# Optimization experiments

Hardware: AMD Instinct MI355X
Metric: run time of the kernel (lower is better)

The kernel has to match this reference:

```python
import jax, jax.numpy as jnp
import numpy as np

GROUP_SIZE = 128  # cfg.group_size

def dequantize_int4(weight_q, scale, zero_point, group_size):
    # weight_q: (out, in) int values in [0,15]; scale/zero_point: (out, n_groups)
    out_f, in_f = weight_q.shape
    n_groups = in_f // group_size
    w = weight_q.astype(jnp.float32).reshape(out_f, n_groups, group_size)
    w = (w - zero_point[:, :, None]) * scale[:, :, None]
    return w.reshape(out_f, in_f)

def setup_inputs() -> dict:
    key = jax.random.key(0)
    k1, k2, k3, k4, k5 = jax.random.split(key, 5)
    B, S, D_IN, D_OUT = 2, 2048, 4096, 4096
    n_groups = D_IN // GROUP_SIZE
    x = jax.random.normal(k1, (B, S, D_IN), dtype=jnp.float32)
    weight_q = jax.random.randint(k2, (D_OUT, D_IN), 0, 16, dtype=jnp.int32)
    scale = jax.random.uniform(k3, (D_OUT, n_groups), dtype=jnp.float32, minval=0.001, maxval=0.02)
    zero_point = jax.random.uniform(k4, (D_OUT, n_groups), dtype=jnp.float32, minval=0.0, maxval=15.0)
    bias = jax.random.normal(k5, (D_OUT,), dtype=jnp.float32)
    return {"x": x, "weight_q": weight_q, "scale": scale, "zero_point": zero_point, "bias": bias}

def reference(x, weight_q, scale, zero_point, bias):
    # Faithful to QuantizedLinear.forward with bits=4: dequantize then F.linear
    w = dequantize_int4(weight_q, scale, zero_point, GROUP_SIZE).astype(x.dtype)  # (out, in)
    return jnp.einsum('bsi,oi->bso', x, w) + bias
```

## Files before the change

### kernel.cpp

```cpp
#include <hip/hip_runtime.h>

typedef __bf16 bf16x8 __attribute__((ext_vector_type(8)));
typedef float f32x4 __attribute__((ext_vector_type(4)));

__device__ __forceinline__ void gload16(const void* g, void* l) {
    __builtin_amdgcn_global_load_lds(
        (const __attribute__((address_space(1))) unsigned int*)g,
        (__attribute__((address_space(3))) unsigned int*)l, 16, 0, 0);
}

__global__ void k_convert_x(const float* __restrict__ x, __bf16* __restrict__ xb, size_t n) {
    size_t i = ((size_t)blockIdx.x * blockDim.x + threadIdx.x) * 8;
    if (i >= n) return;
    const float4 a = *(const float4*)(x + i);
    const float4 b = *(const float4*)(x + i + 4);
    bf16x8 v;
    v[0] = (__bf16)a.x; v[1] = (__bf16)a.y; v[2] = (__bf16)a.z; v[3] = (__bf16)a.w;
    v[4] = (__bf16)b.x; v[5] = (__bf16)b.y; v[6] = (__bf16)b.z; v[7] = (__bf16)b.w;
    *(bf16x8*)(xb + i) = v;
}

__global__ void k_dequant_w(const int* __restrict__ wq, const float* __restrict__ scale,
                            const float* __restrict__ zp, __bf16* __restrict__ wb,
                            int K, int GS, int NG) {
    size_t i = ((size_t)blockIdx.x * blockDim.x + threadIdx.x) * 8;
    int o = (int)(i / K);
    int k = (int)(i % K);
    int g = k / GS;
    float s = scale[(size_t)o * NG + g];
    float z = zp[(size_t)o * NG + g];
    const int4 q0 = *(const int4*)(wq + i);
    const int4 q1 = *(const int4*)(wq + i + 4);
    bf16x8 v;
    v[0] = (__bf16)(((float)q0.x - z) * s); v[1] = (__bf16)(((float)q0.y - z) * s);
    v[2] = (__bf16)(((float)q0.z - z) * s); v[3] = (__bf16)(((float)q0.w - z) * s);
    v[4] = (__bf16)(((float)q1.x - z) * s); v[5] = (__bf16)(((float)q1.y - z) * s);
    v[6] = (__bf16)(((float)q1.z - z) * s); v[7] = (__bf16)(((float)q1.w - z) * s);
    *(bf16x8*)(wb + i) = v;
}

#define BKg 32
#define TILEB 32768
#define ATILEB 16384

__global__ __launch_bounds__(512, 2) void k_gemm256(
    const __bf16* __restrict__ A, const __bf16* __restrict__ B,
    const float* __restrict__ bias, float* __restrict__ C,
    int M, int N, int K)
{
    __shared__ __align__(16) char lds[4 * TILEB];
    const int tid = threadIdx.x;
    const int w = tid >> 6, lane = tid & 63;
    const int wm = w >> 2, wn = w & 3;
    const int lr = lane & 15, hi = lane >> 4;
    const int NT = K / BKg;

    const int nbx = N / 256;
    const int nwg = nbx * (M / 256);
    const int bid = (int)blockIdx.x;
    const int q = nwg >> 3, r = nwg & 7;
    const int xcd = bid & 7, loc = bid >> 3;
    const int swz = (xcd < r ? xcd * (q + 1) : r * (q + 1) + (xcd - r) * q) + loc;
    const int m0 = (swz / nbx) * 256;
    const int n0 = (swz % nbx) * 256;

    size_t aOff[2], bOff[2];
#pragma unroll
    for (int L = 0; L < 2; ++L) {
        int c = L * 512 + tid;
        int row = c >> 2, ch = (c & 3) ^ ((c >> 3) & 3);
        aOff[L] = (size_t)(m0 + row) * K + ch * 8;
        bOff[L] = (size_t)(n0 + row) * K + ch * 8;
    }
    int dstOff[2];
#pragma unroll
    for (int L = 0; L < 2; ++L) dstOff[L] = (L * 512 + w * 64) * 16;

    const int chR = (hi ^ ((lr >> 1) & 3)) * 16;
    const int aRd = (wm * 128 + lr) * 64 + chR;
    const int bRd = ATILEB + (wn * 64 + lr) * 64 + chR;

#define STAGE_A(tt, buf) do {                                              \
    const int kk_ = (tt) * BKg;                                            \
    gload16(A + aOff[0] + kk_, lds + (buf) * TILEB + dstOff[0]);           \
    gload16(A + aOff[1] + kk_, lds + (buf) * TILEB + dstOff[1]);           \
} while (0)
#define STAGE_B(tt, buf) do {                                              \
    const int kk_ = (tt) * BKg;                                            \
    gload16(B + bOff[0] + kk_, lds + (buf) * TILEB + ATILEB + dstOff[0]);  \
    gload16(B + bOff[1] + kk_, lds + (buf) * TILEB + ATILEB + dstOff[1]);  \
} while (0)
#define RD_A(dst, buf, m) dst = *(const bf16x8*)(lds + (buf) * TILEB + aRd + (m) * 1024)
#define RD_B(dst, buf, n) dst = *(const bf16x8*)(lds + (buf) * TILEB + bRd + (n) * 1024)

    f32x4 acc[8][4] = {};
    bf16x8 aF0[8], bF0[4], aF1[8], bF1[4];

    STAGE_A(0, 0); STAGE_B(0, 0);
    STAGE_A(1, 1); STAGE_B(1, 1);
    STAGE_A(2, 2); STAGE_B(2, 2);
    asm volatile("s_waitcnt vmcnt(8)" ::: "memory");
    __builtin_amdgcn_s_barrier();
    RD_A(aF0[0], 0, 0); RD_A(aF0[1], 0, 1); RD_A(aF0[2], 0, 2);
    RD_A(aF0[3], 0, 3); RD_A(aF0[4], 0, 4); RD_A(aF0[5], 0, 5);

#define ITER(t, AC, BC, AN) do {                                            \
    const int bt = (t) & 3, bt1 = ((t) + 1) & 3, bt3 = ((t) + 3) & 3;       \
    int t3 = (t) + 3; if (t3 >= NT) t3 -= NT;                               \
    RD_A(AC[6], bt, 6); RD_A(AC[7], bt, 7);                                 \
    RD_B(BC[0], bt, 0); RD_B(BC[1], bt, 1);                                 \
    RD_B(BC[2], bt, 2); RD_B(BC[3], bt, 3);                                 \
    STAGE_A(t3, bt3);                                                       \
    asm volatile("s_waitcnt vmcnt(6)" ::: "memory");                        \
    __builtin_amdgcn_s_barrier();                                           \
    asm volatile("s_waitcnt lgkmcnt(0)" ::: "memory");                      \
    __builtin_amdgcn_sched_barrier(0);                                      \
    __builtin_amdgcn_s_setprio(1);                                          \
    _Pragma("unroll")                                                       \
    for (int m_ = 0; m_ < 4; ++m_)                                          \
        _Pragma("unroll")                                                   \
        for (int n_ = 0; n_ < 4; ++n_)                                      \
            acc[m_][n_] = __builtin_amdgcn_mfma_f32_16x16x32_bf16(          \
                AC[m_], BC[n_], acc[m_][n_], 0, 0, 0);                      \
    __builtin_amdgcn_s_setprio(0);                                          \
    __builtin_amdgcn_s_barrier();                                           \
    if ((t) + 1 < NT) {                                                     \
        RD_A(AN[0], bt1, 0); RD_A(AN[1], bt1, 1); RD_A(AN[2], bt1, 2);      \
        RD_A(AN[3], bt1, 3); RD_A(AN[4], bt1, 4); RD_A(AN[5], bt1, 5);      \
    }                                                                       \
    STAGE_B(t3, bt3);                                                       \
    __builtin_amdgcn_s_barrier();                                           \
    asm volatile("s_waitcnt lgkmcnt(0)" ::: "memory");                      \
    __builtin_amdgcn_sched_barrier(0);                                      \
    __builtin_amdgcn_s_setprio(1);                                          \
    _Pragma("unroll")                                                       \
    for (int m_ = 4; m_ < 8; ++m_)                                          \
        _Pragma("unroll")                                                   \
        for (int n_ = 0; n_ < 4; ++n_)                                      \
            acc[m_][n_] = __builtin_amdgcn_mfma_f32_16x16x32_bf16(          \
                AC[m_], BC[n_], acc[m_][n_], 0, 0, 0);                      \
    __builtin_amdgcn_s_setprio(0);                                          \
    __builtin_amdgcn_s_barrier();                                           \
} while (0)

    for (int t = 0; t < NT; t += 2) {
        ITER(t,     aF0, bF0, aF1);
        ITER(t + 1, aF1, bF1, aF0);
    }

#pragma unroll
    for (int n_ = 0; n_ < 4; ++n_) {
        const int col = n0 + wn * 64 + n_ * 16 + lr;
        const float bv = bias[col];
#pragma unroll
        for (int m_ = 0; m_ < 8; ++m_) {
            const size_t rbase = (size_t)(m0 + wm * 128 + m_ * 16 + hi * 4) * N + col;
            C[rbase]               = acc[m_][n_][0] + bv;
            C[rbase + N]           = acc[m_][n_][1] + bv;
            C[rbase + 2 * (size_t)N] = acc[m_][n_][2] + bv;
            C[rbase + 3 * (size_t)N] = acc[m_][n_][3] + bv;
        }
    }
#undef ITER
#undef STAGE_A
#undef STAGE_B
#undef RD_A
#undef RD_B
}

template <int MODE>
__global__ __launch_bounds__(256, 2) void k_gemm(
    const __bf16* __restrict__ Ab, const float* __restrict__ Af,
    const __bf16* __restrict__ Bb, const int* __restrict__ Bq,
    const float* __restrict__ scale, const float* __restrict__ zp,
    const float* __restrict__ bias, float* __restrict__ C,
    int M, int N, int K, int NG, int GS)
{
    __shared__ __align__(16) __bf16 As[128 * 32];
    __shared__ __align__(16) __bf16 Bs[128 * 32];

    const int tid  = threadIdx.x;
    const int w    = tid >> 6;
    const int lane = tid & 63;
    const int wm   = w >> 1, wn = w & 1;
    const int m0   = blockIdx.y * 128, n0 = blockIdx.x * 128;
    const int lr   = lane & 15;
    const int lc   = lane >> 4;

    f32x4 acc[4][4] = {};

    for (int kk = 0; kk < K; kk += 32) {
        if constexpr (MODE == 0) {
#pragma unroll
            for (int i = 0; i < 2; i++) {
                int c = i * 256 + tid;
                const __bf16* g = Ab + (size_t)(m0 + (c >> 2)) * K + kk + (c & 3) * 8;
                gload16(g, (char*)As + (i * 256 + w * 64) * 16);
            }
        } else {
            int row = tid >> 1, half = tid & 1;
            const float* g = Af + (size_t)(m0 + row) * K + kk + half * 16;
            float4 f0 = *(const float4*)g;
            float4 f1 = *(const float4*)(g + 4);
            float4 f2 = *(const float4*)(g + 8);
            float4 f3 = *(const float4*)(g + 12);
            bf16x8 v0, v1;
            v0[0] = (__bf16)f0.x; v0[1] = (__bf16)f0.y; v0[2] = (__bf16)f0.z; v0[3] = (__bf16)f0.w;
            v0[4] = (__bf16)f1.x; v0[5] = (__bf16)f1.y; v0[6] = (__bf16)f1.z; v0[7] = (__bf16)f1.w;
            v1[0] = (__bf16)f2.x; v1[1] = (__bf16)f2.y; v1[2] = (__bf16)f2.z; v1[3] = (__bf16)f2.w;
            v1[4] = (__bf16)f3.x; v1[5] = (__bf16)f3.y; v1[6] = (__bf16)f3.z; v1[7] = (__bf16)f3.w;
            *(bf16x8*)(As + row * 32 + half * 16)     = v0;
            *(bf16x8*)(As + row * 32 + half * 16 + 8) = v1;
        }
        if constexpr (MODE <= 1) {
#pragma unroll
            for (int i = 0; i < 2; i++) {
                int c = i * 256 + tid;
                const __bf16* g = Bb + (size_t)(n0 + (c >> 2)) * K + kk + (c & 3) * 8;
                gload16(g, (char*)Bs + (i * 256 + w * 64) * 16);
            }
        } else {
            int row = tid >> 1, half = tid & 1;
            int o = n0 + row;
            int kbase = kk + half * 16;
            int g = kbase / GS;
            float s = scale[(size_t)o * NG + g];
            float z = zp[(size_t)o * NG + g];
            const int* qp = Bq + (size_t)o * K + kbase;
            int4 q0 = *(const int4*)qp;
            int4 q1 = *(const int4*)(qp + 4);
            int4 q2 = *(const int4*)(qp + 8);
            int4 q3 = *(const int4*)(qp + 12);
            bf16x8 v0, v1;
            v0[0] = (__bf16)(((float)q0.x - z) * s); v0[1] = (__bf16)(((float)q0.y - z) * s);
            v0[2] = (__bf16)(((float)q0.z - z) * s); v0[3] = (__bf16)(((float)q0.w - z) * s);
            v0[4] = (__bf16)(((float)q1.x - z) * s); v0[5] = (__bf16)(((float)q1.y - z) * s);
            v0[6] = (__bf16)(((float)q1.z - z) * s); v0[7] = (__bf16)(((float)q1.w - z) * s);
            v1[0] = (__bf16)(((float)q2.x - z) * s); v1[1] = (__bf16)(((float)q2.y - z) * s);
            v1[2] = (__bf16)(((float)q2.z - z) * s); v1[3] = (__bf16)(((float)q2.w - z) * s);
            v1[4] = (__bf16)(((float)q3.x - z) * s); v1[5] = (__bf16)(((float)q3.y - z) * s);
            v1[6] = (__bf16)(((float)q3.z - z) * s); v1[7] = (__bf16)(((float)q3.w - z) * s);
            *(bf16x8*)(Bs + row * 32 + half * 16)     = v0;
            *(bf16x8*)(Bs + row * 32 + half * 16 + 8) = v1;
        }

        __syncthreads();

        bf16x8 af[4], bfm[4];
#pragma unroll
        for (int a = 0; a < 4; a++)
            af[a] = *(const bf16x8*)(As + (wm * 64 + a * 16 + lr) * 32 + lc * 8);
#pragma unroll
        for (int b = 0; b < 4; b++)
            bfm[b] = *(const bf16x8*)(Bs + (wn * 64 + b * 16 + lr) * 32 + lc * 8);
#pragma unroll
        for (int a = 0; a < 4; a++)
#pragma unroll
            for (int b = 0; b < 4; b++)
                acc[a][b] = __builtin_amdgcn_mfma_f32_16x16x32_bf16(af[a], bfm[b], acc[a][b], 0, 0, 0);

        __syncthreads();
    }

#pragma unroll
    for (int b = 0; b < 4; b++) {
        int col = n0 + wn * 64 + b * 16 + lr;
        float bv = bias[col];
#pragma unroll
        for (int a = 0; a < 4; a++) {
            int rbase = m0 + wm * 64 + a * 16 + lc * 4;
#pragma unroll
            for (int r = 0; r < 4; r++)
                C[(size_t)(rbase + r) * N + col] = acc[a][b][r] + bv;
        }
    }
}

extern "C" void kernel_launch(void* const* d_in, const int* in_sizes, int n_in,
                              void* d_out, int out_size, void* d_ws, size_t ws_size,
                              hipStream_t stream) {
    const float* x     = (const float*)d_in[0];
    const int*   wq    = (const int*)d_in[1];
    const float* scale = (const float*)d_in[2];
    const float* zp    = (const float*)d_in[3];
    const float* bias  = (const float*)d_in[4];
    float* out = (float*)d_out;

    const int    N  = in_sizes[4];
    const long   K  = in_sizes[1] / N;
    const long   M  = in_sizes[0] / K;
    const int    NG = in_sizes[2] / N;
    const int    GS = (int)(K / NG);

    const size_t wbytes = (size_t)N * K * sizeof(__bf16);
    const size_t xbytes = (size_t)M * K * sizeof(__bf16);

    char* ws = (char*)d_ws;
    __bf16* wb = (__bf16*)ws;
    __bf16* xb = (__bf16*)(ws + wbytes);

    const bool big = (M % 256 == 0) && (N % 256 == 0) && (K % 64 == 0) && (K / 32 >= 4);

    if (ws_size >= wbytes + xbytes) {
        size_t nx = (size_t)M * K;
        size_t nw = (size_t)N * K;
        k_convert_x<<<(unsigned)((nx / 8 + 255) / 256), 256, 0, stream>>>(x, xb, nx);
        k_dequant_w<<<(unsigned)((nw / 8 + 255) / 256), 256, 0, stream>>>(wq, scale, zp, wb, (int)K, GS, NG);
        if (big) {
            unsigned nwg = (unsigned)((M / 256) * (N / 256));
            k_gemm256<<<nwg, 512, 0, stream>>>(xb, wb, bias, out, (int)M, N, (int)K);
        } else {
            dim3 grid((unsigned)(N / 128), (unsigned)(M / 128)), blk(256);
            k_gemm<0><<<grid, blk, 0, stream>>>(xb, nullptr, wb, nullptr, scale, zp, bias, out,
                                                (int)M, N, (int)K, NG, GS);
        }
    } else if (ws_size >= wbytes) {
        size_t nw = (size_t)N * K;
        dim3 grid((unsigned)(N / 128), (unsigned)(M / 128)), blk(256);
        k_dequant_w<<<(unsigned)((nw / 8 + 255) / 256), 256, 0, stream>>>(wq, scale, zp, wb, (int)K, GS, NG);
        k_gemm<1><<<grid, blk, 0, stream>>>(nullptr, x, wb, nullptr, scale, zp, bias, out,
                                            (int)M, N, (int)K, NG, GS);
    } else {
        dim3 grid((unsigned)(N / 128), (unsigned)(M / 128)), blk(256);
        k_gemm<2><<<grid, blk, 0, stream>>>(nullptr, x, nullptr, wq, scale, zp, bias, out,
                                            (int)M, N, (int)K, NG, GS);
    }
}
```

Baseline: 155.7 us.

## Restructure GEMM main loop LDS fragment prefetch and cut barriers per iteration

Splits the A fragments into two register halves and double-buffers the B fragments, so the next tile's A[0..3] and B reads are issued before the second MFMA half and A[4..7] reads before the first. The main loop drops from four barriers to two and uses partial lgkmcnt waits, letting LDS reads overlap with MFMA work. The cost is a tighter buffer-reuse schedule, where a race on the 4-stage LDS ring would silently corrupt data, and a different register footprint.

```diff
diff --git a/kernel.cpp b/kernel.cpp
--- a/kernel.cpp
+++ b/kernel.cpp
@@ -94,26 +94,26 @@
 #define RD_B(dst, buf, n) dst = *(const bf16x8*)(lds + (buf) * TILEB + bRd + (n) * 1024)
 
     f32x4 acc[8][4] = {};
-    bf16x8 aF0[8], bF0[4], aF1[8], bF1[4];
+    bf16x8 a03[4], a47[4], b0[4], b1[4];
 
     STAGE_A(0, 0); STAGE_B(0, 0);
     STAGE_A(1, 1); STAGE_B(1, 1);
     STAGE_A(2, 2); STAGE_B(2, 2);
     asm volatile("s_waitcnt vmcnt(8)" ::: "memory");
     __builtin_amdgcn_s_barrier();
-    RD_A(aF0[0], 0, 0); RD_A(aF0[1], 0, 1); RD_A(aF0[2], 0, 2);
-    RD_A(aF0[3], 0, 3); RD_A(aF0[4], 0, 4); RD_A(aF0[5], 0, 5);
-
-#define ITER(t, AC, BC, AN) do {                                            \
+    RD_A(a03[0], 0, 0); RD_A(a03[1], 0, 1); RD_A(a03[2], 0, 2); RD_A(a03[3], 0, 3);
+    RD_B(b0[0], 0, 0);  RD_B(b0[1], 0, 1);  RD_B(b0[2], 0, 2);  RD_B(b0[3], 0, 3);
+
+#define ITER(t, BCUR, BNXT) do {                                            \
     const int bt = (t) & 3, bt1 = ((t) + 1) & 3, bt3 = ((t) + 3) & 3;       \
     int t3 = (t) + 3; if (t3 >= NT) t3 -= NT;                               \
-    RD_A(AC[6], bt, 6); RD_A(AC[7], bt, 7);                                 \
-    RD_B(BC[0], bt, 0); RD_B(BC[1], bt, 1);                                 \
-    RD_B(BC[2], bt, 2); RD_B(BC[3], bt, 3);                                 \
+                   \
     STAGE_A(t3, bt3);                                                       \
+    RD_A(a47[0], bt, 4); RD_A(a47[1], bt, 5);                               \
+    RD_A(a47[2], bt, 6); RD_A(a47[3], bt, 7);                               \
     asm volatile("s_waitcnt vmcnt(6)" ::: "memory");                        \
     __builtin_amdgcn_s_barrier();                                           \
-    asm volatile("s_waitcnt lgkmcnt(0)" ::: "memory");                      \
+    asm volatile("s_waitcnt lgkmcnt(4)" ::: "memory");                      \
     __builtin_amdgcn_sched_barrier(0);                                      \
     __builtin_amdgcn_s_setprio(1);                                          \
     _Pragma("unroll")                                                       \
@@ -121,31 +121,37 @@
         _Pragma("unroll")                                                   \
         for (int n_ = 0; n_ < 4; ++n_)                                      \
             acc[m_][n_] = __builtin_amdgcn_mfma_f32_16x16x32_bf16(          \
-                AC[m_], BC[n_], acc[m_][n_], 0, 0, 0);                      \
+                a03[m_], BCUR[n_], acc[m_][n_], 0, 0, 0);                   \
     __builtin_amdgcn_s_setprio(0);                                          \
-    __builtin_amdgcn_s_barrier();                                           \
+          \
+    STAGE_B(t3, bt3);                                                       \
     if ((t) + 1 < NT) {                                                     \
-        RD_A(AN[0], bt1, 0); RD_A(AN[1], bt1, 1); RD_A(AN[2], bt1, 2);      \
-        RD_A(AN[3], bt1, 3); RD_A(AN[4], bt1, 4); RD_A(AN[5], bt1, 5);      \
+        RD_A(a03[0], bt1, 0); RD_A(a03[1], bt1, 1);                         \
+        RD_A(a03[2], bt1, 2); RD_A(a03[3], bt1, 3);                         \
+        RD_B(BNXT[0], bt1, 0); RD_B(BNXT[1], bt1, 1);                       \
+        RD_B(BNXT[2], bt1, 2); RD_B(BNXT[3], bt1, 3);                       \
+        asm volatile("s_waitcnt vmcnt(6)" ::: "memory");                    \
+        __builtin_amdgcn_s_barrier();                                       \
+        asm volatile("s_waitcnt lgkmcnt(8)" ::: "memory");                  \
+    } else {                                                                \
+        asm volatile("s_waitcnt vmcnt(6)" ::: "memory");                    \
+        __builtin_amdgcn_s_barrier();                                       \
+        asm volatile("s_waitcnt lgkmcnt(0)" ::: "memory");                  \
     }                                                                       \
-    STAGE_B(t3, bt3);                                                       \
-    __builtin_amdgcn_s_barrier();                                           \
-    asm volatile("s_waitcnt lgkmcnt(0)" ::: "memory");                      \
     __builtin_amdgcn_sched_barrier(0);                                      \
     __builtin_amdgcn_s_setprio(1);                                          \
     _Pragma("unroll")                                                       \
-    for (int m_ = 4; m_ < 8; ++m_)                                          \
+    for (int m_ = 0; m_ < 4; ++m_)                                          \
         _Pragma("unroll")                                                   \
         for (int n_ = 0; n_ < 4; ++n_)                                      \
-            acc[m_][n_] = __builtin_amdgcn_mfma_f32_16x16x32_bf16(          \
-                AC[m_], BC[n_], acc[m_][n_], 0, 0, 0);                      \
+            acc[m_ + 4][n_] = __builtin_amdgcn_mfma_f32_16x16x32_bf16(      \
+                a47[m_], BCUR[n_], acc[m_ + 4][n_], 0, 0, 0);               \
     __builtin_amdgcn_s_setprio(0);                                          \
-    __builtin_amdgcn_s_barrier();                                           \
 } while (0)
 
     for (int t = 0; t < NT; t += 2) {
-        ITER(t,     aF0, bF0, aF1);
-        ITER(t + 1, aF1, bF1, aF0);
+        ITER(t,     b0, b1);
+        ITER(t + 1, b1, b0);
     }
 
 #pragma unroll
@@ -155,8 +161,8 @@
 #pragma unroll
         for (int m_ = 0; m_ < 8; ++m_) {
             const size_t rbase = (size_t)(m0 + wm * 128 + m_ * 16 + hi * 4) * N + col;
-            C[rbase]               = acc[m_][n_][0] + bv;
-            C[rbase + N]           = acc[m_][n_][1] + bv;
+            C[rbase]                 = acc[m_][n_][0] + bv;
+            C[rbase + N]             = acc[m_][n_][1] + bv;
             C[rbase + 2 * (size_t)N] = acc[m_][n_][2] + bv;
             C[rbase + 3 * (size_t)N] = acc[m_][n_][3] + bv;
         }
```

Result: faster. 152.6 us (-2.0%).
